# Kernel tuning notes

Measured on AMD Instinct MI355X. Metric: run time of the kernel, lower is better.

## Reference

```python
import jax, jax.numpy as jnp
import numpy as np
import math

LOG2PI = math.log(2.0 * math.pi)

def _silu(x):
    return x * jax.nn.sigmoid(x)

def _gru(x, W_ih, W_hh, b_ih, b_hh):
    # x: [B,T,X]; torch nn.GRU single layer, batch_first
    B = x.shape[0]
    H = W_hh.shape[1]
    gi_all = jnp.einsum('btx,gx->btg', x, W_ih) + b_ih  # [B,T,3H] input gates precomputed
    def step(h, gi):
        gh = h @ W_hh.T + b_hh
        i_r, i_z, i_n = jnp.split(gi, 3, axis=-1)
        h_r, h_z, h_n = jnp.split(gh, 3, axis=-1)
        r = jax.nn.sigmoid(i_r + h_r)
        z = jax.nn.sigmoid(i_z + h_z)
        n = jnp.tanh(i_n + r * h_n)
        h_new = (1.0 - z) * n + z * h
        return h_new, h_new
    h0 = jnp.zeros((B, H), x.dtype)
    h_last, h_seq = jax.lax.scan(step, h0, jnp.swapaxes(gi_all, 0, 1))
    return jnp.swapaxes(h_seq, 0, 1), h_last  # [B,T,H], [B,H]

def _A_Q(kappa, sigma, dt):
    A = jnp.exp(-kappa * dt)
    two_k_dt = 2.0 * kappa * dt
    small = (two_k_dt < 1e-6).astype(dt.dtype)
    Q_exact = sigma ** 2 * (1.0 - jnp.exp(-two_k_dt)) / jnp.maximum(2.0 * kappa, 1e-12)
    Q_taylor = sigma ** 2 * dt * (1.0 - kappa * dt + two_k_dt ** 2 / 6.0)
    Q = small * Q_taylor + (1.0 - small) * Q_exact
    return A, Q

def _ou_posterior(m0, s0, mu_k, A_k, Q_k, eps0, eps):
    B, Tm1, C = mu_k.shape
    c0 = m0 + s0 * eps0  # [B,C]
    s0c = jnp.maximum(s0, 1e-12)
    log_q0 = -0.5 * (((c0 - m0) / s0c) ** 2 + 2.0 * jnp.log(s0c) + LOG2PI).sum(-1)
    noise = eps * jnp.sqrt(jnp.maximum(Q_k, 1e-12))
    b = (1.0 - A_k) * mu_k + noise
    Phi_prefix = jnp.cumprod(A_k, axis=1)  # [B,T-1,C]
    Phi_full = jnp.concatenate([jnp.ones((B, 1, C), mu_k.dtype), Phi_prefix], axis=1)
    denom = jnp.maximum(Phi_full[:, 1:, :], 1e-20)
    s = b / denom
    S_full = jnp.concatenate([jnp.zeros((B, 1, C), mu_k.dtype), jnp.cumsum(s, axis=1)], axis=1)
    c = Phi_full * (c0[:, None, :] + S_full)  # [B,T,C]
    mean_trans = mu_k + A_k * (c[:, :-1, :] - mu_k)
    var_trans = jnp.maximum(Q_k, 1e-12)
    log_q_trans = -0.5 * ((c[:, 1:, :] - mean_trans) ** 2 / var_trans + jnp.log(var_trans) + LOG2PI)
    log_q = log_q0 + log_q_trans.sum(-1).sum(-1)
    return c, log_q

def reference(x, t, eps0, eps, W_ih, W_hh, b_ih, b_hh, Wi1, bi1, Wi2, bi2, Ws1, bs1, Ws2, bs2, Ws3, bs3):
    B, T, _ = x.shape
    h_seq, h_global = _gru(x, W_ih, W_hh, b_ih, b_hh)
    # soft time attention, temperature = 1.0
    delta = t[:, :, None, 0] - t[:, None, :, 0]  # [B,T,T]
    logits = -(T * delta) ** 2  # / tau^2 with tau=1
    w = jax.nn.softmax(logits, axis=-1)
    attn = jnp.einsum('bkj,bjh->bkh', w, h_seq)
    # init head
    h0_ctx = h_global + attn[:, 0, :]
    hi = _silu(h0_ctx @ Wi1.T + bi1)
    m0, logs0 = jnp.split(hi @ Wi2.T + bi2, 2, axis=-1)
    s0 = jax.nn.softplus(logs0) + 1e-6
    # step head on ctx[:, :-1]
    ctx = jnp.concatenate([h_global[:, None, :] + attn, t], axis=-1)[:, :-1, :]
    hs = _silu(ctx @ Ws1.T + bs1)
    hs = _silu(hs @ Ws2.T + bs2)
    params = hs @ Ws3.T + bs3
    mu_k, logk_k, logs_k = jnp.split(params, 3, axis=-1)
    kappa_k = jax.nn.softplus(logk_k) + 1e-6
    sigma_k = jax.nn.softplus(logs_k) + 1e-6
    dt = jnp.maximum(t[:, 1:, :] - t[:, :-1, :], 1e-6)
    A_k, Q_k = _A_Q(kappa_k, sigma_k, dt)
    c, log_q = _ou_posterior(m0, s0, mu_k, A_k, Q_k, eps0, eps)
    return c, log_q

def setup_inputs() -> dict:
    B, T, X, H, C = 8, 2048, 64, 256, 32
    key = jax.random.key(0)
    ks = jax.random.split(key, 16)
    def w(k, shape, scale=0.02):
        return (scale * jax.random.normal(k, shape)).astype(jnp.float32)
    x = jax.random.normal(ks[0], (B, T, X), dtype=jnp.float32)
    t = jnp.sort(jax.random.uniform(ks[1], (B, T, 1), dtype=jnp.float32), axis=1)
    eps0 = jax.random.normal(ks[2], (B, C), dtype=jnp.float32)
    eps = jax.random.normal(ks[3], (B, T - 1, C), dtype=jnp.float32)
    return {
        'x': x, 't': t, 'eps0': eps0, 'eps': eps,
        'W_ih': w(ks[4], (3 * H, X)), 'W_hh': w(ks[5], (3 * H, H)),
        'b_ih': jnp.zeros((3 * H,), jnp.float32), 'b_hh': jnp.zeros((3 * H,), jnp.float32),
        'Wi1': w(ks[6], (H, H)), 'bi1': jnp.zeros((H,), jnp.float32),
        'Wi2': w(ks[7], (2 * C, H)), 'bi2': jnp.zeros((2 * C,), jnp.float32),
        'Ws1': w(ks[8], (H, H + 1)), 'bs1': jnp.zeros((H,), jnp.float32),
        'Ws2': w(ks[9], (H, H)), 'bs2': jnp.zeros((H,), jnp.float32),
        'Ws3': w(ks[10], (3 * C, H)), 'bs3': jnp.zeros((3 * C,), jnp.float32),
    }
```

## Files before the change

kernel.cpp:

```cpp
#include <hip/hip_runtime.h>
#include <hip/hip_fp16.h>

#define LOG2PI_F 1.8378770664093453f

typedef _Float16 hf8_t __attribute__((ext_vector_type(8)));
typedef float f32x4_t __attribute__((ext_vector_type(4)));

__device__ __forceinline__ unsigned int packh2(float lo, float hi) {
  unsigned int l = (unsigned int)__half_as_ushort(__float2half(lo));
  unsigned int h = (unsigned int)__half_as_ushort(__float2half(hi));
  return (h << 16) | l;
}

__device__ __forceinline__ float sigmoid_f(float x) { return 1.f / (1.f + __expf(-x)); }
__device__ __forceinline__ float silu_f(float x) { return x * sigmoid_f(x); }
__device__ __forceinline__ float softplus_f(float x) {
  return fmaxf(x, 0.f) + log1pf(__expf(-fabsf(x)));
}
__device__ __forceinline__ float tanh_f(float x) {
  float ax = fabsf(x);
  float e = __expf(2.f * ax);
  return copysignf(1.f - 2.f / (e + 1.f), x);
}

__global__ void transpose_k(const float* __restrict__ in, float* __restrict__ out,
                            int R, int C) {
  int i = blockIdx.x * 256 + threadIdx.x;
  if (i < R * C) {
    int r = i / C, c = i % C;
    out[c * R + r] = in[i];
  }
}

__global__ void whh_mfma_pack(const float* __restrict__ W, unsigned int* __restrict__ Wmf) {
  int idx = blockIdx.x * 256 + threadIdx.x;
  if (idx < 98304) {
    int d = idx & 3;
    int u4 = idx >> 2;
    int lane = u4 & 63;
    int rem = u4 >> 6;
    int kt = rem & 7;
    int mt = rem >> 3;
    int row = 16 * mt + (lane & 15);
    int col = 32 * kt + 8 * (lane >> 4) + 2 * d;
    Wmf[idx] = packh2(W[row * 256 + col], W[row * 256 + col + 1]);
  }
}

__global__ void gi_gemm(const float* __restrict__ x, const float* __restrict__ WT,
                        const float* __restrict__ bih, const float* __restrict__ bhh,
                        float* __restrict__ gi) {
  int m0 = blockIdx.x * 8;
  int g = threadIdx.x;
  __shared__ float xs[8][64];
  for (int i = g; i < 512; i += 256) xs[i >> 6][i & 63] = x[m0 * 64 + i];
  __syncthreads();
  float b0 = bih[g] + bhh[g];
  float b1 = bih[g + 256] + bhh[g + 256];
  float b2 = bih[g + 512];
  float a0[8], a1[8], a2[8];
#pragma unroll
  for (int r = 0; r < 8; r++) { a0[r] = b0; a1[r] = b1; a2[r] = b2; }
  for (int k = 0; k < 64; k++) {
    const float* w = WT + k * 768;
    float w0 = w[g], w1 = w[g + 256], w2 = w[g + 512];
#pragma unroll
    for (int r = 0; r < 8; r++) {
      float xv = xs[r][k];
      a0[r] = fmaf(w0, xv, a0[r]);
      a1[r] = fmaf(w1, xv, a1[r]);
      a2[r] = fmaf(w2, xv, a2[r]);
    }
  }
#pragma unroll
  for (int r = 0; r < 8; r++) {
    float* o = gi + (m0 + r) * 768;
    o[g] = a0[r];
    o[g + 256] = a1[r];
    o[g + 512] = a2[r];
  }
}

__global__ __launch_bounds__(768, 3) void gru_kernel(
    const uint4* __restrict__ Wmf,
    const float* __restrict__ gi,
    const float* __restrict__ bhh,
    float* __restrict__ h_seq)
{
  const int b = blockIdx.x;
  const int tid = threadIdx.x;
  const int w = tid >> 6;
  const int lane = tid & 63;

  uint4 wA[32];
#pragma unroll
  for (int i = 0; i < 32; i++) wA[i] = Wmf[(w * 32 + i) * 64 + lane];

  __shared__ __align__(16) unsigned int hpk[2][128];
  __shared__ __align__(16) float als[768];
  if (tid < 128) hpk[0][tid] = 0u;

  const float* gib = gi + b * 2048 * 768;
  float* hsb = h_seq + b * 2048 * 256;

  float h = 0.f, bn = 0.f, gr = 0.f, gz = 0.f, gn = 0.f;
  if (tid < 256) {
    bn = bhh[512 + tid];
    gr = gib[tid];
    gz = gib[256 + tid];
    gn = gib[512 + tid];
  }
  __syncthreads();

  for (int t = 0; t < 2048; t++) {
    float grn = 0.f, gzn = 0.f, gnn = 0.f;
    if (tid < 256) {
      const float* gnx = gib + min(t + 1, 2047) * 768;
      grn = gnx[tid];
      gzn = gnx[256 + tid];
      gnn = gnx[512 + tid];
    }

    const char* hb = (const char*)(hpk[t & 1]) + 16 * (lane >> 4);
    f32x4_t a0 = {0.f, 0.f, 0.f, 0.f}, a1 = a0, a2 = a0, a3 = a0;
    uint4 hc = *(const uint4*)(hb);
    uint4 hn = *(const uint4*)(hb + 64);
#pragma unroll
    for (int kt = 0; kt < 8; kt++) {
      hf8_t bf = __builtin_bit_cast(hf8_t, hc);
      a0 = __builtin_amdgcn_mfma_f32_16x16x32_f16(
          __builtin_bit_cast(hf8_t, wA[kt]), bf, a0, 0, 0, 0);
      a1 = __builtin_amdgcn_mfma_f32_16x16x32_f16(
          __builtin_bit_cast(hf8_t, wA[8 + kt]), bf, a1, 0, 0, 0);
      a2 = __builtin_amdgcn_mfma_f32_16x16x32_f16(
          __builtin_bit_cast(hf8_t, wA[16 + kt]), bf, a2, 0, 0, 0);
      a3 = __builtin_amdgcn_mfma_f32_16x16x32_f16(
          __builtin_bit_cast(hf8_t, wA[24 + kt]), bf, a3, 0, 0, 0);
      hc = hn;
      if (kt < 6) hn = *(const uint4*)(hb + 64 * (kt + 2));
    }
    if ((lane & 15) == 0) {
      int rbase = 64 * w + 4 * (lane >> 4);
      *(f32x4_t*)&als[rbase] = a0;
      *(f32x4_t*)&als[rbase + 16] = a1;
      *(f32x4_t*)&als[rbase + 32] = a2;
      *(f32x4_t*)&als[rbase + 48] = a3;
    }
    __syncthreads();

    if (tid < 256) {
      float rv = sigmoid_f(als[tid] + gr);
      float zv = sigmoid_f(als[256 + tid] + gz);
      float nv = tanh_f(gn + rv * (als[512 + tid] + bn));
      float hnew = (1.f - zv) * nv + zv * h;
      h = hnew;
      hsb[t * 256 + tid] = hnew;
      float other = __shfl_xor(hnew, 1);
      if ((tid & 1) == 0) hpk[(t + 1) & 1][tid >> 1] = packh2(hnew, other);
    }
    gr = grn;
    gz = gzn;
    gn = gnn;
    __syncthreads();
  }
}

#define AW 80
__global__ void attn_kernel(const float* __restrict__ h_seq, const float* __restrict__ t,
                            float* __restrict__ ctx) {
  const int blk = blockIdx.x;
  const int b = blk >> 7;
  const int k0 = (blk & 127) << 4;
  const int tid = threadIdx.x;

  __shared__ __align__(16) float ewT[176][16];
  __shared__ float ts[176];
  __shared__ float tks[16];
  __shared__ float rden[16];

  const float* tb = t + b * 2048;
  if (tid < 176) {
    int j = k0 - AW + tid;
    ts[tid] = tb[min(max(j, 0), 2047)];
  }
  if (tid < 16) tks[tid] = tb[k0 + tid];
  __syncthreads();

  for (int p = tid; p < 176 * 16; p += 256) {
    int kk = p & 15, jr = p >> 4;
    int j = k0 - AW + jr;
    float d = 2048.f * (tks[kk] - ts[jr]);
    float e = (j >= 0 && j < 2048) ? __expf(-d * d) : 0.f;
    ewT[jr][kk] = e;
  }
  __syncthreads();

  if (tid < 16) {
    float s = 0.f;
    for (int jr = 0; jr < 176; jr++) s += ewT[jr][tid];
    rden[tid] = 1.f / s;
  }
  __syncthreads();

  float acc[16];
#pragma unroll
  for (int kk = 0; kk < 16; kk++) acc[kk] = 0.f;

  const float* hb = h_seq + b * 2048 * 256;
  for (int jr = 0; jr < 176; jr++) {
    int j = min(max(k0 - AW + jr, 0), 2047);
    float hv = hb[j * 256 + tid];
    const float4* e4 = (const float4*)ewT[jr];
    float4 e0 = e4[0], e1 = e4[1], e2 = e4[2], e3 = e4[3];
    acc[0] = fmaf(e0.x, hv, acc[0]);   acc[1] = fmaf(e0.y, hv, acc[1]);
    acc[2] = fmaf(e0.z, hv, acc[2]);   acc[3] = fmaf(e0.w, hv, acc[3]);
    acc[4] = fmaf(e1.x, hv, acc[4]);   acc[5] = fmaf(e1.y, hv, acc[5]);
    acc[6] = fmaf(e1.z, hv, acc[6]);   acc[7] = fmaf(e1.w, hv, acc[7]);
    acc[8] = fmaf(e2.x, hv, acc[8]);   acc[9] = fmaf(e2.y, hv, acc[9]);
    acc[10] = fmaf(e2.z, hv, acc[10]); acc[11] = fmaf(e2.w, hv, acc[11]);
    acc[12] = fmaf(e3.x, hv, acc[12]); acc[13] = fmaf(e3.y, hv, acc[13]);
    acc[14] = fmaf(e3.z, hv, acc[14]); acc[15] = fmaf(e3.w, hv, acc[15]);
  }

  float hg = hb[2047 * 256 + tid];
  float* cb = ctx + (b * 2048 + k0) * 256 + tid;
#pragma unroll
  for (int kk = 0; kk < 16; kk++) cb[kk * 256] = hg + acc[kk] * rden[kk];
}

__global__ void init_head(const float* __restrict__ ctx, const float* __restrict__ WT1,
                          const float* __restrict__ bi1, const float* __restrict__ WT2,
                          const float* __restrict__ bi2, const float* __restrict__ eps0,
                          float* __restrict__ m0s0, float* __restrict__ lq0) {
  int b = blockIdx.x;
  int g = threadIdx.x;
  __shared__ float xs[256], his[256], ms[64], red[32];
  xs[g] = ctx[(b * 2048) * 256 + g];
  __syncthreads();
  float acc = bi1[g];
#pragma unroll 8
  for (int k = 0; k < 256; k++) acc = fmaf(WT1[k * 256 + g], xs[k], acc);
  his[g] = silu_f(acc);
  __syncthreads();
  if (g < 64) {
    float a2 = bi2[g];
#pragma unroll 8
    for (int k = 0; k < 256; k++) a2 = fmaf(WT2[k * 64 + g], his[k], a2);
    float v = (g < 32) ? a2 : (softplus_f(a2) + 1e-6f);
    m0s0[b * 64 + g] = v;
    ms[g] = v;
  }
  __syncthreads();
  if (g < 32) {
    float m = ms[g], s = ms[32 + g];
    float c0 = m + s * eps0[b * 32 + g];
    float sc = fmaxf(s, 1e-12f);
    float z = (c0 - m) / sc;
    red[g] = z * z + 2.f * __logf(sc) + LOG2PI_F;
  }
  __syncthreads();
  if (g == 0) {
    float s = 0.f;
    for (int i = 0; i < 32; i++) s += red[i];
    lq0[b] = -0.5f * s;
  }
}

__global__ void head_layer(const float* __restrict__ A, const float* __restrict__ WT,
                           const float* __restrict__ bias, const float* __restrict__ wext,
                           const float* __restrict__ tvec, float* __restrict__ C,
                           int N, int act) {
  int m0 = blockIdx.x * 8;
  int g = threadIdx.x;
  __shared__ __align__(16) float As[8][256];
#pragma unroll
  for (int r = 0; r < 8; r++) As[r][g] = A[(m0 + r) * 256 + g];
  __syncthreads();
  if (g < N) {
    float b0 = bias[g];
    float acc[8] = {b0, b0, b0, b0, b0, b0, b0, b0};
    for (int k4 = 0; k4 < 64; k4++) {
      const float* w = WT + (k4 * 4) * N + g;
      float w0v = w[0], w1v = w[N], w2v = w[2 * N], w3v = w[3 * N];
#pragma unroll
      for (int r = 0; r < 8; r++) {
        float4 xv = *(const float4*)(&As[r][k4 * 4]);
        acc[r] = fmaf(w0v, xv.x, acc[r]);
        acc[r] = fmaf(w1v, xv.y, acc[r]);
        acc[r] = fmaf(w2v, xv.z, acc[r]);
        acc[r] = fmaf(w3v, xv.w, acc[r]);
      }
    }
#pragma unroll
    for (int r = 0; r < 8; r++) {
      float a = acc[r];
      if (wext) a = fmaf(tvec[m0 + r], wext[g], a);
      if (act) a = silu_f(a);
      C[(m0 + r) * N + g] = a;
    }
  }
}

__global__ __launch_bounds__(1024) void ou_kernel(
    const float* __restrict__ params, const float* __restrict__ t,
    const float* __restrict__ eps, const float* __restrict__ eps0,
    const float* __restrict__ m0s0, const float* __restrict__ lq0,
    float* __restrict__ out) {
  const int b = blockIdx.x;
  const int c = threadIdx.x & 31;
  const int s = threadIdx.x >> 5;
  const int k0 = s * 64;
  const int k1 = min(k0 + 64, 2047);
  const float* tb = t + b * 2048;

  __shared__ float Ps[32][33], Ss[32][33], Cs[32][33], lqs[32][33];

  float P = 1.f, S = 0.f, lq = 0.f;
  for (int k = k0; k < k1; k++) {
    const float* pr = params + (b * 2048 + k) * 96;
    float mu = pr[c];
    float kap = softplus_f(pr[32 + c]) + 1e-6f;
    float sg = softplus_f(pr[64 + c]) + 1e-6f;
    float dt = fmaxf(tb[k + 1] - tb[k], 1e-6f);
    float A = __expf(-kap * dt);
    float tkd = 2.f * kap * dt;
    float Qe = sg * sg * (1.f - A * A) / fmaxf(2.f * kap, 1e-12f);
    float kd = kap * dt;
    float Qt = sg * sg * dt * (1.f - kd + tkd * tkd * (1.f / 6.f));
    float var = fmaxf((tkd < 1e-6f) ? Qt : Qe, 1e-12f);
    float e = eps[(b * 2047 + k) * 32 + c];
    float d = mu * (1.f - A) + e * sqrtf(var);
    S = fmaf(A, S, d);
    P *= A;
    lq += e * e + __logf(var) + LOG2PI_F;
  }
  Ps[c][s] = P;
  Ss[c][s] = S;
  lqs[c][s] = lq;
  __syncthreads();

  if (s == 0) {
    float m0v = m0s0[b * 64 + c];
    float s0v = m0s0[b * 64 + 32 + c];
    float cc = fmaf(s0v, eps0[b * 32 + c], m0v);
    out[(b * 2048) * 32 + c] = cc;
    float lqt = 0.f;
    for (int i = 0; i < 32; i++) {
      Cs[c][i] = cc;
      cc = fmaf(Ps[c][i], cc, Ss[c][i]);
      lqt += lqs[c][i];
    }
    for (int off = 16; off >= 1; off >>= 1) lqt += __shfl_down(lqt, off, 32);
    if (c == 0) out[8 * 2048 * 32 + b] = lq0[b] - 0.5f * lqt;
  }
  __syncthreads();

  float cc = Cs[c][s];
  for (int k = k0; k < k1; k++) {
    const float* pr = params + (b * 2048 + k) * 96;
    float mu = pr[c];
    float kap = softplus_f(pr[32 + c]) + 1e-6f;
    float sg = softplus_f(pr[64 + c]) + 1e-6f;
    float dt = fmaxf(tb[k + 1] - tb[k], 1e-6f);
    float A = __expf(-kap * dt);
    float tkd = 2.f * kap * dt;
    float Qe = sg * sg * (1.f - A * A) / fmaxf(2.f * kap, 1e-12f);
    float kd = kap * dt;
    float Qt = sg * sg * dt * (1.f - kd + tkd * tkd * (1.f / 6.f));
    float var = fmaxf((tkd < 1e-6f) ? Qt : Qe, 1e-12f);
    float e = eps[(b * 2047 + k) * 32 + c];
    float d = mu * (1.f - A) + e * sqrtf(var);
    cc = fmaf(A, cc, d);
    out[(b * 2048 + k + 1) * 32 + c] = cc;
  }
}

extern "C" void kernel_launch(void* const* d_in, const int* in_sizes, int n_in,
                              void* d_out, int out_size, void* d_ws, size_t ws_size,
                              hipStream_t stream) {
  (void)in_sizes; (void)n_in; (void)out_size; (void)ws_size;
  const float* x    = (const float*)d_in[0];
  const float* t    = (const float*)d_in[1];
  const float* eps0 = (const float*)d_in[2];
  const float* eps  = (const float*)d_in[3];
  const float* W_ih = (const float*)d_in[4];
  const float* W_hh = (const float*)d_in[5];
  const float* b_ih = (const float*)d_in[6];
  const float* b_hh = (const float*)d_in[7];
  const float* Wi1  = (const float*)d_in[8];
  const float* bi1  = (const float*)d_in[9];
  const float* Wi2  = (const float*)d_in[10];
  const float* bi2  = (const float*)d_in[11];
  const float* Ws1  = (const float*)d_in[12];
  const float* bs1  = (const float*)d_in[13];
  const float* Ws2  = (const float*)d_in[14];
  const float* bs2  = (const float*)d_in[15];
  const float* Ws3  = (const float*)d_in[16];
  const float* bs3  = (const float*)d_in[17];
  float* out = (float*)d_out;
  float* ws = (float*)d_ws;

  float*        WT_ih = ws + 0;
  unsigned int* Wmf   = (unsigned int*)(ws + 49152);
  float*        WT1   = ws + 147456;
  float*        WT2   = ws + 212992;
  float*        WTs1  = ws + 229376;
  float*        WTs2  = ws + 295168;
  float*        WTs3  = ws + 360704;
  float*        m0s0  = ws + 385280;
  float*        lq0   = ws + 385792;
  float*        gi    = ws + 385800;
  float*        h_seq = gi + 12582912;
  float*        ctx   = h_seq + 4194304;
  float*        hs1    = gi;
  float*        hs2    = gi + 4194304;
  float*        params = gi + 8388608;

  transpose_k<<<(768 * 64 + 255) / 256, 256, 0, stream>>>(W_ih, WT_ih, 768, 64);
  transpose_k<<<(256 * 256 + 255) / 256, 256, 0, stream>>>(Wi1, WT1, 256, 256);
  transpose_k<<<(64 * 256 + 255) / 256, 256, 0, stream>>>(Wi2, WT2, 64, 256);
  transpose_k<<<(256 * 257 + 255) / 256, 256, 0, stream>>>(Ws1, WTs1, 256, 257);
  transpose_k<<<(256 * 256 + 255) / 256, 256, 0, stream>>>(Ws2, WTs2, 256, 256);
  transpose_k<<<(96 * 256 + 255) / 256, 256, 0, stream>>>(Ws3, WTs3, 96, 256);
  whh_mfma_pack<<<384, 256, 0, stream>>>(W_hh, Wmf);

  gi_gemm<<<2048, 256, 0, stream>>>(x, WT_ih, b_ih, b_hh, gi);
  gru_kernel<<<8, 768, 0, stream>>>((const uint4*)Wmf, gi, b_hh, h_seq);
  attn_kernel<<<1024, 256, 0, stream>>>(h_seq, t, ctx);
  init_head<<<8, 256, 0, stream>>>(ctx, WT1, bi1, WT2, bi2, eps0, m0s0, lq0);
  head_layer<<<2048, 256, 0, stream>>>(ctx, WTs1, bs1, WTs1 + 256 * 256, t, hs1, 256, 1);
  head_layer<<<2048, 256, 0, stream>>>(hs1, WTs2, bs2, nullptr, nullptr, hs2, 256, 1);
  head_layer<<<2048, 256, 0, stream>>>(hs2, WTs3, bs3, nullptr, nullptr, params, 96, 0);
  ou_kernel<<<8, 1024, 0, stream>>>(params, t, eps, eps0, m0s0, lq0, out);
}
```

Before: 3.657 ms.

## Restructure GRU recurrence so each wave owns all gates of its hidden units

The W_hh pack and the gi layout are reordered so each of 8 waves holds r, z and n gate rows for the same 32 hidden units (48 weight fragments per lane). Gate nonlinearities are then applied directly on MFMA accumulators in registers, which removes the LDS round trip of gate pre-activations and one of the two block barriers per timestep. In exchange the block drops from 12 to 8 waves and each wave carries more registers and serial MFMA work per step, and the h LDS loads are no longer software-prefetched.

New measurement: 7.101 ms. +94.2%, slower.

```diff
diff --git a/kernel.cpp b/kernel.cpp
--- a/kernel.cpp
+++ b/kernel.cpp
@@ -40,8 +40,11 @@
     int lane = u4 & 63;
     int rem = u4 >> 6;
     int kt = rem & 7;
-    int mt = rem >> 3;
-    int row = 16 * mt + (lane & 15);
+    int mtw = rem >> 3;
+    int mt = mtw % 6;
+    int w = mtw / 6;
+    int g = mt >> 1, half = mt & 1;
+    int row = g * 256 + 32 * w + 16 * half + (lane & 15);
     int col = 32 * kt + 8 * (lane >> 4) + 2 * d;
     Wmf[idx] = packh2(W[row * 256 + col], W[row * 256 + col + 1]);
   }
@@ -72,16 +75,17 @@
       a2[r] = fmaf(w2, xv, a2[r]);
     }
   }
+  int wv = g >> 5, l = g & 31;
 #pragma unroll
   for (int r = 0; r < 8; r++) {
-    float* o = gi + (m0 + r) * 768;
-    o[g] = a0[r];
-    o[g + 256] = a1[r];
-    o[g + 512] = a2[r];
-  }
-}
-
-__global__ __launch_bounds__(768, 3) void gru_kernel(
+    float* o = gi + (m0 + r) * 768 + wv * 96;
+    o[l] = a0[r];
+    o[32 + l] = a1[r];
+    o[64 + l] = a2[r];
+  }
+}
+
+__global__ __launch_bounds__(512, 1) void gru_kernel(
     const uint4* __restrict__ Wmf,
     const float* __restrict__ gi,
     const float* __restrict__ bhh,
@@ -91,43 +95,51 @@
   const int tid = threadIdx.x;
   const int w = tid >> 6;
   const int lane = tid & 63;
-
-  uint4 wA[32];
-#pragma unroll
-  for (int i = 0; i < 32; i++) wA[i] = Wmf[(w * 32 + i) * 64 + lane];
+  const int q = lane >> 4;
+
+  uint4 wA[48];
+#pragma unroll
+  for (int i = 0; i < 48; i++) wA[i] = Wmf[(w * 48 + i) * 64 + lane];
 
   __shared__ __align__(16) unsigned int hpk[2][128];
-  __shared__ __align__(16) float als[768];
   if (tid < 128) hpk[0][tid] = 0u;
+
+  const int dbase = 32 * w + 4 * q;
+  float bn0[4], bn1[4], h0[4], h1[4];
+#pragma unroll
+  for (int e = 0; e < 4; e++) {
+    bn0[e] = bhh[512 + dbase + e];
+    bn1[e] = bhh[512 + dbase + 16 + e];
+    h0[e] = 0.f;
+    h1[e] = 0.f;
+  }
 
   const float* gib = gi + b * 2048 * 768;
   float* hsb = h_seq + b * 2048 * 256;
-
-  float h = 0.f, bn = 0.f, gr = 0.f, gz = 0.f, gn = 0.f;
-  if (tid < 256) {
-    bn = bhh[512 + tid];
-    gr = gib[tid];
-    gz = gib[256 + tid];
-    gn = gib[512 + tid];
-  }
-  __syncthreads();
-
+  const float* gw0 = gib + w * 96 + 4 * q;
+  float4 gr0 = *(const float4*)(gw0 + 0);
+  float4 gr1 = *(const float4*)(gw0 + 16);
+  float4 gz0 = *(const float4*)(gw0 + 32);
+  float4 gz1 = *(const float4*)(gw0 + 48);
+  float4 gn0 = *(const float4*)(gw0 + 64);
+  float4 gn1 = *(const float4*)(gw0 + 80);
+  __syncthreads();
+
+  int cur = 0;
   for (int t = 0; t < 2048; t++) {
-    float grn = 0.f, gzn = 0.f, gnn = 0.f;
-    if (tid < 256) {
-      const float* gnx = gib + min(t + 1, 2047) * 768;
-      grn = gnx[tid];
-      gzn = gnx[256 + tid];
-      gnn = gnx[512 + tid];
-    }
-
-    const char* hb = (const char*)(hpk[t & 1]) + 16 * (lane >> 4);
-    f32x4_t a0 = {0.f, 0.f, 0.f, 0.f}, a1 = a0, a2 = a0, a3 = a0;
-    uint4 hc = *(const uint4*)(hb);
-    uint4 hn = *(const uint4*)(hb + 64);
+    const float* gnx = gib + min(t + 1, 2047) * 768 + w * 96 + 4 * q;
+    float4 pr0 = *(const float4*)(gnx + 0);
+    float4 pr1 = *(const float4*)(gnx + 16);
+    float4 pz0 = *(const float4*)(gnx + 32);
+    float4 pz1 = *(const float4*)(gnx + 48);
+    float4 pn0 = *(const float4*)(gnx + 64);
+    float4 pn1 = *(const float4*)(gnx + 80);
+
+    const char* hb = (const char*)hpk[cur] + 16 * q;
+    f32x4_t a0 = {0.f, 0.f, 0.f, 0.f}, a1 = a0, a2 = a0, a3 = a0, a4 = a0, a5 = a0;
 #pragma unroll
     for (int kt = 0; kt < 8; kt++) {
-      hf8_t bf = __builtin_bit_cast(hf8_t, hc);
+      hf8_t bf = __builtin_bit_cast(hf8_t, *(const uint4*)(hb + 64 * kt));
       a0 = __builtin_amdgcn_mfma_f32_16x16x32_f16(
           __builtin_bit_cast(hf8_t, wA[kt]), bf, a0, 0, 0, 0);
       a1 = __builtin_amdgcn_mfma_f32_16x16x32_f16(
@@ -136,32 +148,47 @@
           __builtin_bit_cast(hf8_t, wA[16 + kt]), bf, a2, 0, 0, 0);
       a3 = __builtin_amdgcn_mfma_f32_16x16x32_f16(
           __builtin_bit_cast(hf8_t, wA[24 + kt]), bf, a3, 0, 0, 0);
-      hc = hn;
-      if (kt < 6) hn = *(const uint4*)(hb + 64 * (kt + 2));
-    }
+      a4 = __builtin_amdgcn_mfma_f32_16x16x32_f16(
+          __builtin_bit_cast(hf8_t, wA[32 + kt]), bf, a4, 0, 0, 0);
+      a5 = __builtin_amdgcn_mfma_f32_16x16x32_f16(
+          __builtin_bit_cast(hf8_t, wA[40 + kt]), bf, a5, 0, 0, 0);
+    }
+
+    {
+      float rv, zv, nv;
+      rv = sigmoid_f(a0[0] + gr0.x); zv = sigmoid_f(a2[0] + gz0.x);
+      nv = tanh_f(gn0.x + rv * (a4[0] + bn0[0])); h0[0] = (1.f - zv) * nv + zv * h0[0];
+      rv = sigmoid_f(a0[1] + gr0.y); zv = sigmoid_f(a2[1] + gz0.y);
+      nv = tanh_f(gn0.y + rv * (a4[1] + bn0[1])); h0[1] = (1.f - zv) * nv + zv * h0[1];
+      rv = sigmoid_f(a0[2] + gr0.z); zv = sigmoid_f(a2[2] + gz0.z);
+      nv = tanh_f(gn0.z + rv * (a4[2] + bn0[2])); h0[2] = (1.f - zv) * nv + zv * h0[2];
+      rv = sigmoid_f(a0[3] + gr0.w); zv = sigmoid_f(a2[3] + gz0.w);
+      nv = tanh_f(gn0.w + rv * (a4[3] + bn0[3])); h0[3] = (1.f - zv) * nv + zv * h0[3];
+
+      rv = sigmoid_f(a1[0] + gr1.x); zv = sigmoid_f(a3[0] + gz1.x);
+      nv = tanh_f(gn1.x + rv * (a5[0] + bn1[0])); h1[0] = (1.f - zv) * nv + zv * h1[0];
+      rv = sigmoid_f(a1[1] + gr1.y); zv = sigmoid_f(a3[1] + gz1.y);
+      nv = tanh_f(gn1.y + rv * (a5[1] + bn1[1])); h1[1] = (1.f - zv) * nv + zv * h1[1];
+      rv = sigmoid_f(a1[2] + gr1.z); zv = sigmoid_f(a3[2] + gz1.z);
+      nv = tanh_f(gn1.z + rv * (a5[2] + bn1[2])); h1[2] = (1.f - zv) * nv + zv * h1[2];
+      rv = sigmoid_f(a1[3] + gr1.w); zv = sigmoid_f(a3[3] + gz1.w);
+      nv = tanh_f(gn1.w + rv * (a5[3] + bn1[3])); h1[3] = (1.f - zv) * nv + zv * h1[3];
+    }
+
     if ((lane & 15) == 0) {
-      int rbase = 64 * w + 4 * (lane >> 4);
-      *(f32x4_t*)&als[rbase] = a0;
-      *(f32x4_t*)&als[rbase + 16] = a1;
-      *(f32x4_t*)&als[rbase + 32] = a2;
-      *(f32x4_t*)&als[rbase + 48] = a3;
-    }
+      float4 v0 = {h0[0], h0[1], h0[2], h0[3]};
+      float4 v1 = {h1[0], h1[1], h1[2], h1[3]};
+      *(float4*)&hsb[t * 256 + dbase] = v0;
+      *(float4*)&hsb[t * 256 + dbase + 16] = v1;
+      uint2 p0 = {packh2(h0[0], h0[1]), packh2(h0[2], h0[3])};
+      uint2 p1 = {packh2(h1[0], h1[1]), packh2(h1[2], h1[3])};
+      *(uint2*)&hpk[cur ^ 1][16 * w + 2 * q] = p0;
+      *(uint2*)&hpk[cur ^ 1][16 * w + 8 + 2 * q] = p1;
+    }
+
+    gr0 = pr0; gr1 = pr1; gz0 = pz0; gz1 = pz1; gn0 = pn0; gn1 = pn1;
     __syncthreads();
-
-    if (tid < 256) {
-      float rv = sigmoid_f(als[tid] + gr);
-      float zv = sigmoid_f(als[256 + tid] + gz);
-      float nv = tanh_f(gn + rv * (als[512 + tid] + bn));
-      float hnew = (1.f - zv) * nv + zv * h;
-      h = hnew;
-      hsb[t * 256 + tid] = hnew;
-      float other = __shfl_xor(hnew, 1);
-      if ((tid & 1) == 0) hpk[(t + 1) & 1][tid >> 1] = packh2(hnew, other);
-    }
-    gr = grn;
-    gz = gzn;
-    gn = gnn;
-    __syncthreads();
+    cur ^= 1;
   }
 }
 
@@ -422,10 +449,10 @@
   transpose_k<<<(256 * 257 + 255) / 256, 256, 0, stream>>>(Ws1, WTs1, 256, 257);
   transpose_k<<<(256 * 256 + 255) / 256, 256, 0, stream>>>(Ws2, WTs2, 256, 256);
   transpose_k<<<(96 * 256 + 255) / 256, 256, 0, stream>>>(Ws3, WTs3, 96, 256);
-  whh_mfma_pack<<<384, 256, 0, stream>>>(W_hh, Wmf);
+  whh_mfma_pack<<<384, 256, 0, stream>>>(W_hh, (unsigned int*)Wmf);
 
   gi_gemm<<<2048, 256, 0, stream>>>(x, WT_ih, b_ih, b_hh, gi);
-  gru_kernel<<<8, 768, 0, stream>>>((const uint4*)Wmf, gi, b_hh, h_seq);
+  gru_kernel<<<8, 512, 0, stream>>>((const uint4*)Wmf, gi, b_hh, h_seq);
   attn_kernel<<<1024, 256, 0, stream>>>(h_seq, t, ctx);
   init_head<<<8, 256, 0, stream>>>(ctx, WT1, bi1, WT2, bi2, eps0, m0s0, lq0);
   head_layer<<<2048, 256, 0, stream>>>(ctx, WTs1, bs1, WTs1 + 256 * 256, t, hs1, 256, 1);
```
